# Performance work log

Measured on AMD Instinct MI355X. Metric: run time of the kernel, lower is better.

## Reference

```python
import jax, jax.numpy as jnp
import numpy as np

B, FIN, FOUT, FH2, NMIX, LAT, H, W = 16, 256, 256, 256, 8, 512, 64, 64


def _xavier(key, shape):
    # xavier_normal_ over last-two-ish dims; simple fan-based scale
    fan_in = int(np.prod(shape[1:]))
    fan_out = shape[0]
    s = (2.0 / (fan_in + fan_out)) ** 0.5
    return jax.random.normal(key, shape, jnp.float32) * s


def setup_inputs() -> dict:
    key = jax.random.key(0)
    ks = jax.random.split(key, 12)
    return {
        "x": jax.random.normal(ks[0], (B, FIN, H, W), jnp.float32),
        "lat": jax.random.normal(ks[1], (B, LAT), jnp.float32),
        # mixture kernel banks [n_mix, out_ch, in_ch] (kernel_size=1 squeezed)
        "k_in_mix": _xavier(ks[2], (NMIX, FH2, FIN)),
        "k_mid_mix": _xavier(ks[3], (NMIX, FH2, 2 * FH2)),
        "k_out_mix": _xavier(ks[4], (NMIX, FOUT, 2 * FH2)),
        "k_short_mix": _xavier(ks[5], (NMIX, FOUT, FIN)),
        # mixture bias banks [n_mix, ch]
        "b_in_mix": _xavier(ks[6], (NMIX, FH2)),
        "b_mid_mix": _xavier(ks[7], (NMIX, FH2)),
        "b_out_mix": _xavier(ks[8], (NMIX, FOUT)),
        "b_short_mix": _xavier(ks[9], (NMIX, FOUT)),
        # dyna_mix = nn.Linear(lat_size, n_mix) (lat_factor=0 path)
        "w_dyna": _xavier(ks[10], (NMIX, LAT)),
        "b_dyna": jnp.zeros((NMIX,), jnp.float32),
    }


def _complex_wave(h):
    # doubles channel dim: concat(sin, cos) along channels (per sample)
    return jnp.concatenate([jnp.sin(h), jnp.cos(h)], axis=1)


def reference(x, lat, k_in_mix, k_mid_mix, k_out_mix, k_short_mix,
              b_in_mix, b_mid_mix, b_out_mix, b_short_mix, w_dyna, b_dyna):
    # mixing coefficients per sample: [B, n_mix]
    mix = lat @ w_dyna.T + b_dyna
    # per-sample 1x1 conv kernels via mixture reduction: [B, out, in]
    k_in = jnp.einsum('bm,moi->boi', mix, k_in_mix)
    k_mid = jnp.einsum('bm,moi->boi', mix, k_mid_mix)
    k_out = jnp.einsum('bm,moi->boi', mix, k_out_mix)
    k_short = jnp.einsum('bm,moi->boi', mix, k_short_mix)
    # per-sample biases: [B, ch, 1, 1]
    b_in = (mix @ b_in_mix)[:, :, None, None]
    b_mid = (mix @ b_mid_mix)[:, :, None, None]
    b_out = (mix @ b_out_mix)[:, :, None, None]
    b_short = (mix @ b_short_mix)[:, :, None, None]
    # grouped conv with groups = batch (kernel_size=1) == per-sample matmul
    short = jnp.einsum('boi,bihw->bohw', k_short, x) + b_short
    h = jnp.einsum('boi,bihw->bohw', k_in, x) + b_in            # [B, FH2, H, W]
    h = _complex_wave(h)                                        # [B, 2*FH2, H, W]
    h = jnp.einsum('boi,bihw->bohw', k_mid, h) + b_mid
    h = _complex_wave(h)
    out = jnp.einsum('boi,bihw->bohw', k_out, h) + b_out + short
    return out
```

## Files before the change

### kernel.cpp

```cpp
#include <hip/hip_runtime.h>
#include <stdint.h>

#define B_    16
#define FIN   256
#define FOUT  256
#define FH2   256
#define NMIX  8
#define LAT   512
#define HW    4096
#define MT    32

typedef short bf16x8 __attribute__((ext_vector_type(8)));
typedef float f32x4  __attribute__((ext_vector_type(4)));

#define WS_MIX    0
#define WS_BIAS   1024
#define WS_WIN    131072
#define WS_WMID   2228224
#define WS_WOUT   6422528
#define WS_WSHORT 10616832

__device__ __forceinline__ uint16_t f2bf(float f) {
  uint32_t u = __builtin_bit_cast(uint32_t, f);
  u += 0x7fffu + ((u >> 16) & 1u);
  return (uint16_t)(u >> 16);
}
__device__ __forceinline__ uint32_t pack2(float lo, float hi) {
  return (uint32_t)f2bf(lo) | ((uint32_t)f2bf(hi) << 16);
}

#define MFMA(a, b, c) __builtin_amdgcn_mfma_f32_16x16x32_bf16(a, b, c, 0, 0, 0)

__global__ void k_mix_bias(const float* __restrict__ lat,
                           const float* __restrict__ w_dyna,
                           const float* __restrict__ b_dyna,
                           const float* __restrict__ b_in_mix,
                           const float* __restrict__ b_mid_mix,
                           const float* __restrict__ b_out_mix,
                           const float* __restrict__ b_short_mix,
                           float* __restrict__ ws_mix,
                           float* __restrict__ ws_bias) {
  __shared__ float smix[NMIX];
  const int t = threadIdx.x;
  const int lane = t & 63, wv = t >> 6;
  const int b = blockIdx.x;
#pragma unroll
  for (int d2 = 0; d2 < 2; d2++) {
    int m = wv * 2 + d2;
    float s = 0.f;
#pragma unroll
    for (int j = 0; j < 8; j++)
      s += lat[b * LAT + j * 64 + lane] * w_dyna[m * LAT + j * 64 + lane];
#pragma unroll
    for (int off = 32; off; off >>= 1) s += __shfl_xor(s, off);
    if (lane == 0) {
      float v = s + b_dyna[m];
      ws_mix[b * NMIX + m] = v;
      smix[m] = v;
    }
  }
  __syncthreads();
  const float* banks[4] = {b_in_mix, b_mid_mix, b_out_mix, b_short_mix};
  for (int pos = t; pos < 1024; pos += 256) {
    int bank = pos >> 8, ch = pos & 255;
    const float* bp = banks[bank];
    float a = 0.f;
#pragma unroll
    for (int m = 0; m < NMIX; m++) a += smix[m] * bp[m * 256 + ch];
    ws_bias[(bank * B_ + b) * 256 + ch] = a;
  }
}

__global__ void k_weights(const float* __restrict__ k_in_mix,
                          const float* __restrict__ k_mid_mix,
                          const float* __restrict__ k_out_mix,
                          const float* __restrict__ k_short_mix,
                          const float* __restrict__ ws_mix,
                          uint16_t* __restrict__ w_in,
                          uint16_t* __restrict__ w_mid,
                          uint16_t* __restrict__ w_out,
                          uint16_t* __restrict__ w_short) {
  __shared__ float smix[B_ * NMIX];
  const int t = threadIdx.x;
  if (t < B_ * NMIX) smix[t] = ws_mix[t];
  __syncthreads();
  const int idx = blockIdx.x * 256 + t;
  const float* src;
  uint16_t* dst;
  int sstride, dstride;
  if (idx < 65536) {
    int e = idx;
    int j = e & 7, lane = (e >> 3) & 63, ots = (e >> 9) & 3, kt = (e >> 11) & 7, wv = e >> 14;
    int row = wv * 64 + ots * 16 + (lane & 15);
    int k = kt * 32 + (lane >> 4) * 8 + j;
    src = k_in_mix + row * 256 + k; sstride = 65536;
    dst = w_in + e;                 dstride = 65536;
  } else if (idx < 196608) {
    int e = idx - 65536;
    int j = e & 7, lane = (e >> 3) & 63, ots = (e >> 9) & 3, kt = (e >> 11) & 15, wv = e >> 15;
    int row = wv * 64 + ots * 16 + (lane & 15);
    int kp = kt * 32 + (lane >> 4) * 8 + j;
    int i = (kp >> 1) + ((kp & 1) << 8);
    src = k_mid_mix + row * 512 + i; sstride = 131072;
    dst = w_mid + e;                 dstride = 131072;
  } else if (idx < 327680) {
    int e = idx - 196608;
    int j = e & 7, lane = (e >> 3) & 63, ots = (e >> 9) & 3, kt = (e >> 11) & 15, wv = e >> 15;
    int row = wv * 64 + ots * 16 + (lane & 15);
    int kp = kt * 32 + (lane >> 4) * 8 + j;
    int i = (kp >> 1) + ((kp & 1) << 8);
    src = k_out_mix + row * 512 + i; sstride = 131072;
    dst = w_out + e;                 dstride = 131072;
  } else {
    int e = idx - 327680;
    int j = e & 7, lane = (e >> 3) & 63, ots = (e >> 9) & 3, kt = (e >> 11) & 7, wv = e >> 14;
    int row = wv * 64 + ots * 16 + (lane & 15);
    int k = kt * 32 + (lane >> 4) * 8 + j;
    src = k_short_mix + row * 256 + k; sstride = 65536;
    dst = w_short + e;                 dstride = 65536;
  }
  float v[NMIX];
#pragma unroll
  for (int m = 0; m < NMIX; m++) v[m] = src[m * sstride];
  for (int b = 0; b < B_; b++) {
    float a = 0.f;
#pragma unroll
    for (int m = 0; m < NMIX; m++) a += smix[b * NMIX + m] * v[m];
    dst[b * dstride] = f2bf(a);
  }
}

__launch_bounds__(256, 3)
__global__ void k_main(const float* __restrict__ x,
                       const float* __restrict__ ws_bias,
                       const uint16_t* __restrict__ w_in,
                       const uint16_t* __restrict__ w_mid,
                       const uint16_t* __restrict__ w_out,
                       const uint16_t* __restrict__ w_short,
                       float* __restrict__ out) {
  __shared__ int4 smem4[49152 / 16];
  char* lds = (char*)smem4;
  char* Xb = lds;
  char* H1 = lds + 16384;
  char* H2 = lds;

  const int t = threadIdx.x;
  const int lane = t & 63;
  const int wv = t >> 6;
  const int q = lane >> 4;
  const int n = lane & 15;
  const int b = blockIdx.x & 15;
  const int p0 = (blockIdx.x >> 4) * MT;

  {
    const float* xb = x + (size_t)b * FIN * HW + p0;
    const int p = t & 31;
    const int cg = t >> 5;
#pragma unroll
    for (int cc = 0; cc < 4; cc++) {
      int c = cg * 4 + cc;
      float v[8];
#pragma unroll
      for (int e = 0; e < 8; e++) v[e] = xb[(size_t)(c * 8 + e) * HW + p];
      int4 pkt = make_int4((int)pack2(v[0], v[1]), (int)pack2(v[2], v[3]),
                           (int)pack2(v[4], v[5]), (int)pack2(v[6], v[7]));
      *(int4*)(Xb + p * 512 + ((c ^ (p & 7)) * 16)) = pkt;
    }
  }
  __syncthreads();

  f32x4 acc_h[4][2], acc_s[4][2];
#pragma unroll
  for (int ots = 0; ots < 4; ots++) {
    int o = wv * 64 + ots * 16 + q * 4;
    float4 vi = *(const float4*)&ws_bias[(0 * B_ + b) * 256 + o];
    float4 vs = *(const float4*)&ws_bias[(3 * B_ + b) * 256 + o];
    acc_h[ots][0][0] = vi.x; acc_h[ots][0][1] = vi.y; acc_h[ots][0][2] = vi.z; acc_h[ots][0][3] = vi.w;
    acc_h[ots][1] = acc_h[ots][0];
    acc_s[ots][0][0] = vs.x; acc_s[ots][0][1] = vs.y; acc_s[ots][0][2] = vs.z; acc_s[ots][0][3] = vs.w;
    acc_s[ots][1] = acc_s[ots][0];
  }
  {
    const uint16_t* Wi = w_in + (size_t)b * 65536 + wv * 16384 + lane * 8;
    const uint16_t* Ws = w_short + (size_t)b * 65536 + wv * 16384 + lane * 8;
#pragma unroll
    for (int kt = 0; kt < 8; kt++) {
      int sw = ((kt * 4 + q) ^ (n & 7)) * 16;
      bf16x8 bf0 = *(const bf16x8*)(Xb + n * 512 + sw);
      bf16x8 bf1 = *(const bf16x8*)(Xb + (16 + n) * 512 + sw);
#pragma unroll
      for (int ots = 0; ots < 4; ots++) {
        bf16x8 ai = *(const bf16x8*)(Wi + kt * 2048 + ots * 512);
        bf16x8 as = *(const bf16x8*)(Ws + kt * 2048 + ots * 512);
        acc_h[ots][0] = MFMA(ai, bf0, acc_h[ots][0]);
        acc_h[ots][1] = MFMA(ai, bf1, acc_h[ots][1]);
        acc_s[ots][0] = MFMA(as, bf0, acc_s[ots][0]);
        acc_s[ots][1] = MFMA(as, bf1, acc_s[ots][1]);
      }
    }
  }
#pragma unroll
  for (int ots = 0; ots < 4; ots++) {
    int ctile = (wv * 4 + ots) * 4 + q;
#pragma unroll
    for (int pt = 0; pt < 2; pt++) {
      int p = pt * 16 + n;
      uint32_t u0 = pack2(__sinf(acc_h[ots][pt][0]), __cosf(acc_h[ots][pt][0]));
      uint32_t u1 = pack2(__sinf(acc_h[ots][pt][1]), __cosf(acc_h[ots][pt][1]));
      uint32_t u2 = pack2(__sinf(acc_h[ots][pt][2]), __cosf(acc_h[ots][pt][2]));
      uint32_t u3 = pack2(__sinf(acc_h[ots][pt][3]), __cosf(acc_h[ots][pt][3]));
      *(int4*)(H1 + p * 1024 + ((ctile ^ (p & 7)) * 16)) =
          make_int4((int)u0, (int)u1, (int)u2, (int)u3);
    }
  }
  __syncthreads();

  f32x4 acc2[4][2];
#pragma unroll
  for (int ots = 0; ots < 4; ots++) {
    int o = wv * 64 + ots * 16 + q * 4;
    float4 v = *(const float4*)&ws_bias[(1 * B_ + b) * 256 + o];
    acc2[ots][0][0] = v.x; acc2[ots][0][1] = v.y; acc2[ots][0][2] = v.z; acc2[ots][0][3] = v.w;
    acc2[ots][1] = acc2[ots][0];
  }
  {
    const uint16_t* Wm = w_mid + (size_t)b * 131072 + wv * 32768 + lane * 8;
#pragma unroll
    for (int kt = 0; kt < 16; kt++) {
      int sw = ((kt * 4 + q) ^ (n & 7)) * 16;
      bf16x8 bf0 = *(const bf16x8*)(H1 + n * 1024 + sw);
      bf16x8 bf1 = *(const bf16x8*)(H1 + (16 + n) * 1024 + sw);
#pragma unroll
      for (int ots = 0; ots < 4; ots++) {
        bf16x8 am = *(const bf16x8*)(Wm + kt * 2048 + ots * 512);
        acc2[ots][0] = MFMA(am, bf0, acc2[ots][0]);
        acc2[ots][1] = MFMA(am, bf1, acc2[ots][1]);
      }
    }
  }
  __syncthreads();
#pragma unroll
  for (int ots = 0; ots < 4; ots++) {
    int ctile = (wv * 4 + ots) * 4 + q;
#pragma unroll
    for (int pt = 0; pt < 2; pt++) {
      int p = pt * 16 + n;
      uint32_t u0 = pack2(__sinf(acc2[ots][pt][0]), __cosf(acc2[ots][pt][0]));
      uint32_t u1 = pack2(__sinf(acc2[ots][pt][1]), __cosf(acc2[ots][pt][1]));
      uint32_t u2 = pack2(__sinf(acc2[ots][pt][2]), __cosf(acc2[ots][pt][2]));
      uint32_t u3 = pack2(__sinf(acc2[ots][pt][3]), __cosf(acc2[ots][pt][3]));
      *(int4*)(H2 + p * 1024 + ((ctile ^ (p & 7)) * 16)) =
          make_int4((int)u0, (int)u1, (int)u2, (int)u3);
    }
  }
  __syncthreads();

  f32x4 acc3[4][2];
#pragma unroll
  for (int ots = 0; ots < 4; ots++) {
    int o = wv * 64 + ots * 16 + q * 4;
    float4 v = *(const float4*)&ws_bias[(2 * B_ + b) * 256 + o];
    acc3[ots][0][0] = acc_s[ots][0][0] + v.x; acc3[ots][0][1] = acc_s[ots][0][1] + v.y;
    acc3[ots][0][2] = acc_s[ots][0][2] + v.z; acc3[ots][0][3] = acc_s[ots][0][3] + v.w;
    acc3[ots][1][0] = acc_s[ots][1][0] + v.x; acc3[ots][1][1] = acc_s[ots][1][1] + v.y;
    acc3[ots][1][2] = acc_s[ots][1][2] + v.z; acc3[ots][1][3] = acc_s[ots][1][3] + v.w;
  }
  {
    const uint16_t* Wo = w_out + (size_t)b * 131072 + wv * 32768 + lane * 8;
#pragma unroll
    for (int kt = 0; kt < 16; kt++) {
      int sw = ((kt * 4 + q) ^ (n & 7)) * 16;
      bf16x8 bf0 = *(const bf16x8*)(H2 + n * 1024 + sw);
      bf16x8 bf1 = *(const bf16x8*)(H2 + (16 + n) * 1024 + sw);
#pragma unroll
      for (int ots = 0; ots < 4; ots++) {
        bf16x8 ao = *(const bf16x8*)(Wo + kt * 2048 + ots * 512);
        acc3[ots][0] = MFMA(ao, bf0, acc3[ots][0]);
        acc3[ots][1] = MFMA(ao, bf1, acc3[ots][1]);
      }
    }
  }
  {
    float* ob = out + (size_t)b * FOUT * HW + p0;
#pragma unroll
    for (int ots = 0; ots < 4; ots++) {
#pragma unroll
      for (int pt = 0; pt < 2; pt++) {
#pragma unroll
        for (int r = 0; r < 4; r++) {
          int o = wv * 64 + ots * 16 + q * 4 + r;
          ob[(size_t)o * HW + pt * 16 + n] = acc3[ots][pt][r];
        }
      }
    }
  }
}

extern "C" void kernel_launch(void* const* d_in, const int* in_sizes, int n_in,
                              void* d_out, int out_size, void* d_ws, size_t ws_size,
                              hipStream_t stream) {
  const float* x           = (const float*)d_in[0];
  const float* lat         = (const float*)d_in[1];
  const float* k_in_mix    = (const float*)d_in[2];
  const float* k_mid_mix   = (const float*)d_in[3];
  const float* k_out_mix   = (const float*)d_in[4];
  const float* k_short_mix = (const float*)d_in[5];
  const float* b_in_mix    = (const float*)d_in[6];
  const float* b_mid_mix   = (const float*)d_in[7];
  const float* b_out_mix   = (const float*)d_in[8];
  const float* b_short_mix = (const float*)d_in[9];
  const float* w_dyna      = (const float*)d_in[10];
  const float* b_dyna      = (const float*)d_in[11];

  char* ws = (char*)d_ws;
  float*    ws_mix  = (float*)(ws + WS_MIX);
  float*    ws_bias = (float*)(ws + WS_BIAS);
  uint16_t* w_in    = (uint16_t*)(ws + WS_WIN);
  uint16_t* w_mid   = (uint16_t*)(ws + WS_WMID);
  uint16_t* w_out   = (uint16_t*)(ws + WS_WOUT);
  uint16_t* w_short = (uint16_t*)(ws + WS_WSHORT);
  float* out = (float*)d_out;

  hipLaunchKernelGGL(k_mix_bias, dim3(16), dim3(256), 0, stream,
                     lat, w_dyna, b_dyna, b_in_mix, b_mid_mix, b_out_mix,
                     b_short_mix, ws_mix, ws_bias);
  hipLaunchKernelGGL(k_weights, dim3(1536), dim3(256), 0, stream,
                     k_in_mix, k_mid_mix, k_out_mix, k_short_mix, ws_mix,
                     w_in, w_mid, w_out, w_short);
  hipLaunchKernelGGL(k_main, dim3(2048), dim3(256), 0, stream,
                     x, ws_bias, w_in, w_mid, w_out, w_short, out);
}
```

Baseline: 234.1 us.

## Fuse mix/bias prep into weight kernel and shrink main kernel LDS

Merges the mixing-coefficient/bias kernel into the weight-mixing kernel. Every block now recomputes all 128 mixing coefficients redundantly with a serial 512-length dot product per thread, which removes one launch. Separately, the main kernel aliases H1 onto the X buffer (adding a barrier) to cut LDS from 48KB to 32KB, and raises launch bounds to 5 blocks per SM for occupancy. The risks are the redundant serial mix computation in 1536 blocks and tighter register limits.

```diff
diff --git a/kernel.cpp b/kernel.cpp
--- a/kernel.cpp
+++ b/kernel.cpp
@@ -13,7 +13,6 @@
 typedef short bf16x8 __attribute__((ext_vector_type(8)));
 typedef float f32x4  __attribute__((ext_vector_type(4)));
 
-#define WS_MIX    0
 #define WS_BIAS   1024
 #define WS_WIN    131072
 #define WS_WMID   2228224
@@ -31,59 +30,48 @@
 
 #define MFMA(a, b, c) __builtin_amdgcn_mfma_f32_16x16x32_bf16(a, b, c, 0, 0, 0)
 
-__global__ void k_mix_bias(const float* __restrict__ lat,
-                           const float* __restrict__ w_dyna,
-                           const float* __restrict__ b_dyna,
-                           const float* __restrict__ b_in_mix,
-                           const float* __restrict__ b_mid_mix,
-                           const float* __restrict__ b_out_mix,
-                           const float* __restrict__ b_short_mix,
-                           float* __restrict__ ws_mix,
-                           float* __restrict__ ws_bias) {
-  __shared__ float smix[NMIX];
-  const int t = threadIdx.x;
-  const int lane = t & 63, wv = t >> 6;
-  const int b = blockIdx.x;
-#pragma unroll
-  for (int d2 = 0; d2 < 2; d2++) {
-    int m = wv * 2 + d2;
-    float s = 0.f;
-#pragma unroll
-    for (int j = 0; j < 8; j++)
-      s += lat[b * LAT + j * 64 + lane] * w_dyna[m * LAT + j * 64 + lane];
-#pragma unroll
-    for (int off = 32; off; off >>= 1) s += __shfl_xor(s, off);
-    if (lane == 0) {
-      float v = s + b_dyna[m];
-      ws_mix[b * NMIX + m] = v;
-      smix[m] = v;
-    }
-  }
-  __syncthreads();
-  const float* banks[4] = {b_in_mix, b_mid_mix, b_out_mix, b_short_mix};
-  for (int pos = t; pos < 1024; pos += 256) {
-    int bank = pos >> 8, ch = pos & 255;
-    const float* bp = banks[bank];
-    float a = 0.f;
-#pragma unroll
-    for (int m = 0; m < NMIX; m++) a += smix[m] * bp[m * 256 + ch];
-    ws_bias[(bank * B_ + b) * 256 + ch] = a;
-  }
-}
-
-__global__ void k_weights(const float* __restrict__ k_in_mix,
-                          const float* __restrict__ k_mid_mix,
-                          const float* __restrict__ k_out_mix,
-                          const float* __restrict__ k_short_mix,
-                          const float* __restrict__ ws_mix,
-                          uint16_t* __restrict__ w_in,
-                          uint16_t* __restrict__ w_mid,
-                          uint16_t* __restrict__ w_out,
-                          uint16_t* __restrict__ w_short) {
+__global__ void k_prep(const float* __restrict__ lat,
+                       const float* __restrict__ w_dyna,
+                       const float* __restrict__ b_dyna,
+                       const float* __restrict__ b_in_mix,
+                       const float* __restrict__ b_mid_mix,
+                       const float* __restrict__ b_out_mix,
+                       const float* __restrict__ b_short_mix,
+                       const float* __restrict__ k_in_mix,
+                       const float* __restrict__ k_mid_mix,
+                       const float* __restrict__ k_out_mix,
+                       const float* __restrict__ k_short_mix,
+                       float* __restrict__ ws_bias,
+                       uint16_t* __restrict__ w_in,
+                       uint16_t* __restrict__ w_mid,
+                       uint16_t* __restrict__ w_out,
+                       uint16_t* __restrict__ w_short) {
   __shared__ float smix[B_ * NMIX];
   const int t = threadIdx.x;
-  if (t < B_ * NMIX) smix[t] = ws_mix[t];
-  __syncthreads();
+  if (t < B_ * NMIX) {
+    int b = t >> 3, m = t & 7;
+    float s = 0.f;
+    for (int l = 0; l < LAT; l++) s += lat[b * LAT + l] * w_dyna[m * LAT + l];
+    smix[t] = s + b_dyna[m];
+  }
+  __syncthreads();
+  if (blockIdx.x < 4) {
+    const float* banks[4] = {b_in_mix, b_mid_mix, b_out_mix, b_short_mix};
+    const float* bp = banks[blockIdx.x];
+    int ch = t;
+    if (ch < 256) {
+      float v[NMIX];
+#pragma unroll
+      for (int m = 0; m < NMIX; m++) v[m] = bp[m * 256 + ch];
+#pragma unroll
+      for (int b = 0; b < B_; b++) {
+        float a = 0.f;
+#pragma unroll
+        for (int m = 0; m < NMIX; m++) a += smix[b * NMIX + m] * v[m];
+        ws_bias[(blockIdx.x * B_ + b) * 256 + ch] = a;
+      }
+    }
+  }
   const int idx = blockIdx.x * 256 + t;
   const float* src;
   uint16_t* dst;
@@ -130,7 +118,7 @@
   }
 }
 
-__launch_bounds__(256, 3)
+__launch_bounds__(256, 5)
 __global__ void k_main(const float* __restrict__ x,
                        const float* __restrict__ ws_bias,
                        const uint16_t* __restrict__ w_in,
@@ -138,10 +126,10 @@
                        const uint16_t* __restrict__ w_out,
                        const uint16_t* __restrict__ w_short,
                        float* __restrict__ out) {
-  __shared__ int4 smem4[49152 / 16];
+  __shared__ int4 smem4[32768 / 16];
   char* lds = (char*)smem4;
   char* Xb = lds;
-  char* H1 = lds + 16384;
+  char* H1 = lds;
   char* H2 = lds;
 
   const int t = threadIdx.x;
@@ -199,6 +187,7 @@
       }
     }
   }
+  __syncthreads();
 #pragma unroll
   for (int ots = 0; ots < 4; ots++) {
     int ctile = (wv * 4 + ots) * 4 + q;
@@ -313,7 +302,6 @@
   const float* b_dyna      = (const float*)d_in[11];
 
   char* ws = (char*)d_ws;
-  float*    ws_mix  = (float*)(ws + WS_MIX);
   float*    ws_bias = (float*)(ws + WS_BIAS);
   uint16_t* w_in    = (uint16_t*)(ws + WS_WIN);
   uint16_t* w_mid   = (uint16_t*)(ws + WS_WMID);
@@ -321,12 +309,10 @@
   uint16_t* w_short = (uint16_t*)(ws + WS_WSHORT);
   float* out = (float*)d_out;
 
-  hipLaunchKernelGGL(k_mix_bias, dim3(16), dim3(256), 0, stream,
+  hipLaunchKernelGGL(k_prep, dim3(1536), dim3(256), 0, stream,
                      lat, w_dyna, b_dyna, b_in_mix, b_mid_mix, b_out_mix,
-                     b_short_mix, ws_mix, ws_bias);
-  hipLaunchKernelGGL(k_weights, dim3(1536), dim3(256), 0, stream,
-                     k_in_mix, k_mid_mix, k_out_mix, k_short_mix, ws_mix,
-                     w_in, w_mid, w_out, w_short);
+                     b_short_mix, k_in_mix, k_mid_mix, k_out_mix, k_short_mix,
+                     ws_bias, w_in, w_mid, w_out, w_short);
   hipLaunchKernelGGL(k_main, dim3(2048), dim3(256), 0, stream,
                      x, ws_bias, w_in, w_mid, w_out, w_short, out);
 }
```

After: 349.3 us. +49.2%, slower.
